# Kernel tuning notes

Hardware: AMD Instinct MI355X
Metric: run time of the kernel (lower is better)

Reference implementation:

```python
import jax, jax.numpy as jnp
import numpy as np

EPS_COS = 1e-8   # torch F.cosine_similarity eps
EPS_LN = 1e-6    # LayerNorm eps from source


def _attn_block(x, spat, roi, W, b, k):
    """MultiHeadedAttention_3 (flag=1) forward.
    x: [B,N,C], spat: [B,N,2], roi: [B,N,N], W: [h, 2C+4], b: [h].
    query[b,i,j]=x[b,j], key[b,i,j]=x[b,i]; ft = cat(query,key,spat_q,spat_k).
    The linear over the concat is split into per-part einsums (same math,
    avoids materializing the [B,N,N,2C+4] tensor).
    Returns attn1 * roi * topk-scatter mask, shape [B,N,N,h] (dims b,i,j,h).
    """
    B, N, C = x.shape
    Wq, Wk = W[:, :C], W[:, C:2 * C]
    Wsq, Wsk = W[:, 2 * C:2 * C + 2], W[:, 2 * C + 2:]
    qt = jnp.einsum('bjc,hc->bjh', x, Wq) + jnp.einsum('bjs,hs->bjh', spat, Wsq)
    kt = jnp.einsum('bic,hc->bih', x, Wk) + jnp.einsum('bis,hs->bih', spat, Wsk)
    logits = qt[:, None, :, :] + kt[:, :, None, :] + b  # [B,i,j,h]
    attn1 = jax.nn.sigmoid(logits)
    # relu(cosine_similarity(query, key, dim=3)) -> [B,i,j] (symmetric)
    xn = x / jnp.maximum(jnp.linalg.norm(x, axis=-1, keepdims=True), EPS_COS)
    scores = jax.nn.relu(jnp.einsum('bic,bjc->bij', xn, xn))
    # torch: atten_mask[:, :, idces, :] = 1.0 with idces [B,N,k,1] sets, for ALL
    # b,i,h, column j to 1 whenever j appears anywhere in idces (global scatter).
    _, idx = jax.lax.top_k(scores, k)  # [B,N,k]
    present = jnp.zeros((N,), x.dtype).at[idx.reshape(-1)].set(1.0)
    return attn1 * roi[:, :, :, None] * present[None, None, :, None]


def _gconv_relu(x, w, bias):
    """Grouped 1x1 Conv1d + ReLU. x: [B,Cin,N], w: [g, Cout/g, Cin/g]."""
    B, Cin, N = x.shape
    g, og, ig = w.shape
    y = jnp.einsum('bgin,goi->bgon', x.reshape(B, g, ig, N), w)
    return jax.nn.relu(y.reshape(B, g * og, N) + bias[None, :, None])


def _forward(input, masks_roi, score_mask, spat, W1, b1, W2, b2,
             cw1, cb1, cw2, cb2, ln_g, ln_b, node_num):
    B, N, C = input.shape
    h = W1.shape[0]
    masks = masks_roi * score_mask[:, None, :]
    f = (score_mask == 0).astype(input.dtype)          # [B,N]
    f_mask = f[:, :, None] * jnp.eye(N, dtype=input.dtype)  # diag_embed

    A1 = (_attn_block(input, spat, masks, W1, b1, node_num)
          + f_mask[:, :, :, None]) / 4.0               # [B,i,j,h]

    out1 = _gconv_relu(jnp.swapaxes(input, 1, 2), cw1, cb1)  # [B,mid,N]
    mid = out1.shape[1]
    # torch: matmul(out1.view(B,h,mid/h,N), A1.permute(0,3,2,1))  ([B,h,j,i])
    out1m = jnp.einsum('bhdj,bijh->bhdi', out1.reshape(B, h, mid // h, N), A1)
    out1 = out1 + out1m.reshape(B, mid, N)

    x2 = jnp.swapaxes(out1, 1, 2)                      # [B,N,mid]
    A2 = (_attn_block(x2, spat, masks, W2, b2, node_num)
          + f_mask[:, :, :, None]) / 4.0

    out2 = _gconv_relu(out1, cw2, cb2)                 # [B,out,N]
    co = out2.shape[1]
    out2m = jnp.einsum('bhdj,bijh->bhdi', out2.reshape(B, h, co // h, N), A2)
    out2m = jnp.swapaxes(out2m.reshape(B, co, N), 1, 2)  # [B,N,out]
    mu = jnp.mean(out2m, axis=-1, keepdims=True)
    var = jnp.mean(jnp.square(out2m - mu), axis=-1, keepdims=True)
    out2m = (out2m - mu) / jnp.sqrt(var + EPS_LN) * ln_g + ln_b
    out2 = out2 + jnp.swapaxes(out2m, 1, 2)
    return jnp.swapaxes(out2, 1, 2)                    # [B,N,out]


def setup_inputs() -> dict:
    key = jax.random.key(0)
    ks = jax.random.split(key, 10)
    B, N, C, MID, OUT, H, G = 8, 1024, 256, 256, 256, 4, 4
    s = 0.05
    return {
        'input': jax.random.normal(ks[0], (B, N, C), jnp.float32),
        'masks_roi': jax.random.randint(ks[1], (B, N, N), 0, 2).astype(jnp.float32),
        'score_mask': jax.random.randint(ks[2], (B, N), 0, 2).astype(jnp.float32),
        'spat': jax.random.uniform(ks[3], (B, N, 2), jnp.float32),
        'W1': s * jax.random.normal(ks[4], (H, 2 * C + 4), jnp.float32),
        'b1': jnp.zeros((H,), jnp.float32),
        'W2': s * jax.random.normal(ks[5], (H, 2 * MID + 4), jnp.float32),
        'b2': jnp.zeros((H,), jnp.float32),
        'cw1': s * jax.random.normal(ks[6], (G, MID // G, C // G), jnp.float32),
        'cb1': jnp.zeros((MID,), jnp.float32),
        'cw2': s * jax.random.normal(ks[7], (G, OUT // G, MID // G), jnp.float32),
        'cb2': jnp.zeros((OUT,), jnp.float32),
        'ln_g': jnp.ones((OUT,), jnp.float32),
        'ln_b': jnp.zeros((OUT,), jnp.float32),
        'node_num': 16,
    }


def reference(input, masks_roi, score_mask, spat, W1, b1, W2, b2,
              cw1, cb1, cw2, cb2, ln_g, ln_b, node_num):
    return _forward(input, masks_roi, score_mask, spat, W1, b1, W2, b2,
                    cw1, cb1, cw2, cb2, ln_g, ln_b, node_num)
```

## Files before the change

kernel.cpp:

```cpp
#include <hip/hip_runtime.h>

constexpr int Bb = 8;
constexpr int Nn = 1024;
constexpr int Cc = 256;
constexpr int Hh = 4;
constexpr int WROW = 2 * Cc + 4;

typedef float fx4 __attribute__((ext_vector_type(4)));
typedef float f32x4 __attribute__((ext_vector_type(4)));
typedef __bf16 bf16x8 __attribute__((ext_vector_type(8)));

#define GLL16(src, dst)                                                      \
  __builtin_amdgcn_global_load_lds(                                          \
      (const __attribute__((address_space(1))) void*)(src),                  \
      (__attribute__((address_space(3))) void*)(dst), 16, 0, 0)

__global__ __launch_bounds__(256) void k_roipack2(const float* __restrict__ roi,
                                                  const float* __restrict__ sm,
                                                  unsigned long long* __restrict__ roib,
                                                  int* __restrict__ cntb) {
  __shared__ short jmapS[1024];
  __shared__ unsigned char m4S[4][256];
  __shared__ int cntS;
  const int t = threadIdx.x, w = t >> 6, l = t & 63;
  const int gid = blockIdx.x * 4 + w;
  const int b = gid >> 10;

  if (w == 0) {
    int base = 0;
#pragma unroll
    for (int jc = 0; jc < 16; ++jc) {
      const int j = jc * 64 + l;
      const bool act = sm[b * Nn + j] != 0.f;
      const unsigned long long m = __ballot(act);
      if (act) jmapS[base + __popcll(m & ((1ull << l) - 1))] = (short)j;
      base += __popcll(m);
    }
    if (l == 0) {
      cntS = base;
      if ((blockIdx.x & 255) == 0) cntb[b] = base;
    }
  }

  {
    const fx4* r4 = (const fx4*)(roi + (size_t)gid * Nn);
#pragma unroll
    for (int k = 0; k < 4; ++k) {
      fx4 v = r4[k * 64 + l];
      unsigned nb = (v[0] != 0.f ? 1u : 0u) | (v[1] != 0.f ? 2u : 0u) |
                    (v[2] != 0.f ? 4u : 0u) | (v[3] != 0.f ? 8u : 0u);
      m4S[w][k * 64 + l] = (unsigned char)nb;
    }
  }
  __syncthreads();

  const int cnt = cntS;
  unsigned long long* orow = roib + (size_t)gid * 16;
#pragma unroll 4
  for (int pc = 0; pc < 16; ++pc) {
    const int idx = pc * 64 + l;
    const bool valid = idx < cnt;
    const int j = valid ? (int)jmapS[idx] : 0;
    const bool bit = valid && ((m4S[w][j >> 2] >> (j & 3)) & 1);
    unsigned long long m = __ballot(bit);
    if (l == 0) orow[pc] = m;
  }
}

template <int STAGE>
__global__ __launch_bounds__(256) void k_gconvq(const float* __restrict__ src,
                                                const float* __restrict__ cw,
                                                const float* __restrict__ cb,
                                                const float* __restrict__ sm,
                                                const float* __restrict__ spat,
                                                const float* __restrict__ W,
                                                const float* __restrict__ bias,
                                                float* __restrict__ out,
                                                __bf16* __restrict__ gsm,
                                                float* __restrict__ qt,
                                                float* __restrict__ kt) {
  __shared__ __align__(16) bf16x8 xsB[32][32];
  __shared__ float cbS[256];
  __shared__ float smS[32];
  __shared__ int pcolS[32];
  __shared__ int actS[32];
  const int b = blockIdx.x, tile = blockIdx.y;
  const int n0 = tile * 32;
  const int t = threadIdx.x, w = t >> 6, l = t & 63;

  if (w == 0) {
    const int fullc = n0 >> 6;
    int cbase = 0;
    unsigned long long am = 0;
    for (int jc = 0; jc <= fullc; ++jc) {
      unsigned long long m = __ballot(sm[b * Nn + jc * 64 + l] != 0.f);
      if (jc < fullc) cbase += __popcll(m); else am = m;
    }
    const int lsel = l - (n0 & 63);
    if (lsel >= 0 && lsel < 32) {
      pcolS[lsel] = cbase + __popcll(am & ((1ull << l) - 1));
      actS[lsel] = (int)((am >> l) & 1);
      smS[lsel] = 0.25f * sm[b * Nn + n0 + lsel];
    }
  }
  cbS[t] = cb[t];

  if (STAGE == 0) {
    const int n = t >> 3, c0 = (t & 7) * 32;
    const float* srow = src + ((size_t)(b * Nn + n0 + n)) * Cc + c0;
#pragma unroll
    for (int k = 0; k < 4; ++k) {
      fx4 v0 = *(const fx4*)&srow[k * 8];
      fx4 v1 = *(const fx4*)&srow[k * 8 + 4];
      bf16x8 bv;
#pragma unroll
      for (int e = 0; e < 4; ++e) { bv[e] = (__bf16)v0[e]; bv[4 + e] = (__bf16)v1[e]; }
      xsB[n][((c0 >> 3) + k) ^ (n & 7)] = bv;
    }
  } else {
#pragma unroll
    for (int rr = 0; rr < 8; ++rr) {
      const int c = rr * 32 + (t >> 3);
      const int nq = (t & 7) * 4;
      fx4 v = *(const fx4*)&src[((size_t)(b * Cc + c)) * Nn + n0 + nq];
#pragma unroll
      for (int j = 0; j < 4; ++j) {
        const int n = nq + j;
        __bf16* row = (__bf16*)&xsB[n][(c >> 3) ^ (n & 7)];
        row[c & 7] = (__bf16)v[j];
      }
    }
  }
  __syncthreads();

  const int g = w, dl = l & 15, q = l >> 4;

  bf16x8 a[4][2];
#pragma unroll
  for (int of = 0; of < 4; ++of)
#pragma unroll
    for (int ks = 0; ks < 2; ++ks) {
      const float* cwp = cw + ((size_t)(g * 64 + of * 16 + dl)) * 64 + ks * 32 + q * 8;
      fx4 c0 = *(const fx4*)cwp;
      fx4 c1 = *(const fx4*)(cwp + 4);
#pragma unroll
      for (int e = 0; e < 4; ++e) { a[of][ks][e] = (__bf16)c0[e]; a[of][ks][4 + e] = (__bf16)c1[e]; }
    }
  f32x4 acc[4][2] = {};
#pragma unroll
  for (int nf = 0; nf < 2; ++nf) {
    const int n = nf * 16 + dl;
#pragma unroll
    for (int ks = 0; ks < 2; ++ks) {
      bf16x8 bv = xsB[n][(g * 8 + ks * 4 + q) ^ (n & 7)];
#pragma unroll
      for (int of = 0; of < 4; ++of)
        acc[of][nf] = __builtin_amdgcn_mfma_f32_16x16x32_bf16(a[of][ks], bv, acc[of][nf], 0, 0, 0);
    }
  }
#pragma unroll
  for (int of = 0; of < 4; ++of)
#pragma unroll
    for (int nf = 0; nf < 2; ++nf) {
      const int n = nf * 16 + dl;
      const float smv = smS[n];
      const int act = actS[n];
      const int pc = pcolS[n];
#pragma unroll
      for (int r = 0; r < 4; ++r) {
        const int co = g * 64 + of * 16 + 4 * q + r;
        const float val = fmaxf(acc[of][nf][r] + cbS[co], 0.f);
        const size_t orow = ((size_t)(b * Cc + co)) * Nn;
        out[orow + n0 + n] = val;
        if (act) gsm[orow + pc] = (__bf16)(smv * val);
      }
    }

  {
    const int nl = l & 31, half = l >> 5;
    const float* wq = W + g * WROW;
    const float* wk = wq + Cc;
    float qa = 0.f, ka = 0.f;
#pragma unroll 8
    for (int c2 = 0; c2 < 64; ++c2) {
      const int c = half * 128 + c2 * 2;
      const __bf16* p = (const __bf16*)&xsB[nl][(c >> 3) ^ (nl & 7)] + (c & 7);
      const float x0 = (float)p[0], x1 = (float)p[1];
      qa = fmaf(x0, wq[c], fmaf(x1, wq[c + 1], qa));
      ka = fmaf(x0, wk[c], fmaf(x1, wk[c + 1], ka));
    }
    qa += __shfl_xor(qa, 32, 64);
    ka += __shfl_xor(ka, 32, 64);
    if (l < 32) {
      const int n = n0 + nl;
      const float s0 = spat[(b * Nn + n) * 2 + 0];
      const float s1 = spat[(b * Nn + n) * 2 + 1];
      const float* wsp = W + g * WROW + 2 * Cc;
      const float qf = qa + s0 * wsp[0] + s1 * wsp[1] + bias[g];
      const float kf = ka + s0 * wsp[2] + s1 * wsp[3];
      kt[(b * Hh + g) * Nn + n] = kf * -1.44269504f;
      if (actS[nl]) qt[(b * Hh + g) * Nn + pcolS[nl]] = qf * -1.44269504f;
    }
  }
}

template <int MODE>
__global__ __launch_bounds__(512, 4) void k_apply7(const float* __restrict__ g,
                                                   const __bf16* __restrict__ gsm,
                                                   const float* __restrict__ qt,
                                                   const float* __restrict__ kt,
                                                   const unsigned char* __restrict__ roib,
                                                   const float* __restrict__ sm,
                                                   const int* __restrict__ cntb,
                                                   float* __restrict__ out) {
  __shared__ __align__(16) __bf16 Bs[2][3][2][2048];
  __shared__ __align__(16) float qts[1024];
  __shared__ __align__(16) unsigned char rbs[64 * 128];
  const int b = blockIdx.x, it = blockIdx.y, h = blockIdx.z;
  const int t = threadIdx.x, w = t >> 6, l = t & 63;
  const int grp = w >> 2, wq = w & 3;
  const int i0 = it * 64;
  const int dl = l & 15, q = l >> 4, jqf = q * 8;
  const int iA = i0 + wq * 16 + dl;

  const float kvn = kt[(b * Hh + h) * Nn + iA];
  const float* smrow = sm + b * Nn;

  const int cnt = cntb[b];
  const int stepsTot = (cnt + 63) >> 6;
  const int S = (stepsTot + 1) >> 1;
  const int c0 = grp * S;

  const __bf16* gsrc = gsm + ((size_t)(b * Cc + h * 64 + wq * 16 + (l >> 2))) * Nn
                       + c0 * 64 + (l & 3) * 8;
  __bf16* ring = &Bs[grp][0][0][0];
  const int wdst = wq * 512;

  {
    const float2 qv = *(const float2*)&qt[(b * Hh + h) * Nn + t * 2];
    qts[t * 2 + 0] = qv.x;
    qts[t * 2 + 1] = qv.y;
  }
  {
    const int r = t >> 3, c = (t & 7) * 16;
    const char* src = (const char*)roib + ((size_t)(b * Nn + i0 + r)) * 128 + c;
    *(int4*)&rbs[r * 128 + c] = *(const int4*)src;
  }
  GLL16(gsrc, ring + 0 * 4096 + 0 * 2048 + wdst);
  GLL16(gsrc + 32, ring + 0 * 4096 + 1 * 2048 + wdst);
  GLL16(gsrc + 64, ring + 1 * 4096 + 0 * 2048 + wdst);
  GLL16(gsrc + 96, ring + 1 * 4096 + 1 * 2048 + wdst);
  __syncthreads();

  const int rbbase = (wq * 16 + dl) * 128;
  f32x4 acc[4] = {};
  int cur = 0;

  for (int s = 0; s < S; ++s) {
    const int ck = c0 + s;
    const unsigned int rb0 = rbs[rbbase + ck * 8 + q];
    const unsigned int rb1 = rbs[rbbase + ck * 8 + 4 + q];
    bf16x8 af0, af1;
    {
      fx4 qa = *(const fx4*)&qts[ck * 64 + jqf];
      fx4 qb = *(const fx4*)&qts[ck * 64 + jqf + 4];
#pragma unroll
      for (int e = 0; e < 4; ++e) {
        float sg = __builtin_amdgcn_rcpf(1.f + __builtin_amdgcn_exp2f(qa[e] + kvn));
        af0[e] = (__bf16)(((rb0 >> e) & 1) ? sg : 0.f);
      }
#pragma unroll
      for (int e = 0; e < 4; ++e) {
        float sg = __builtin_amdgcn_rcpf(1.f + __builtin_amdgcn_exp2f(qb[e] + kvn));
        af0[4 + e] = (__bf16)(((rb0 >> (4 + e)) & 1) ? sg : 0.f);
      }
      fx4 qc = *(const fx4*)&qts[ck * 64 + 32 + jqf];
      fx4 qd = *(const fx4*)&qts[ck * 64 + 32 + jqf + 4];
#pragma unroll
      for (int e = 0; e < 4; ++e) {
        float sg = __builtin_amdgcn_rcpf(1.f + __builtin_amdgcn_exp2f(qc[e] + kvn));
        af1[e] = (__bf16)(((rb1 >> e) & 1) ? sg : 0.f);
      }
#pragma unroll
      for (int e = 0; e < 4; ++e) {
        float sg = __builtin_amdgcn_rcpf(1.f + __builtin_amdgcn_exp2f(qd[e] + kvn));
        af1[4 + e] = (__bf16)(((rb1 >> (4 + e)) & 1) ? sg : 0.f);
      }
    }
    asm volatile("s_waitcnt vmcnt(2)\n\ts_barrier" ::: "memory");
    __builtin_amdgcn_sched_barrier(0);
    {
      const int nc = s + 2;
      const int off = (nc < S) ? nc * 64 : 0;
      const int pf = (cur == 0) ? 2 : cur - 1;
      GLL16(gsrc + off, ring + pf * 4096 + 0 * 2048 + wdst);
      GLL16(gsrc + off + 32, ring + pf * 4096 + 1 * 2048 + wdst);
    }
    const __bf16* bp = ring + cur * 4096;
#pragma unroll
    for (int nf = 0; nf < 4; ++nf) {
      bf16x8 bv = *(const bf16x8*)(bp + (nf * 16 + dl) * 32 + jqf);
      acc[nf] = __builtin_amdgcn_mfma_f32_16x16x32_bf16(af0, bv, acc[nf], 0, 0, 0);
    }
#pragma unroll
    for (int nf = 0; nf < 4; ++nf) {
      bf16x8 bv = *(const bf16x8*)(bp + 2048 + (nf * 16 + dl) * 32 + jqf);
      acc[nf] = __builtin_amdgcn_mfma_f32_16x16x32_bf16(af1, bv, acc[nf], 0, 0, 0);
    }
    cur = (cur == 2) ? 0 : cur + 1;
  }

  __syncthreads();
  float* accS = (float*)&Bs[0][0][0][0];
  if (grp == 1) {
#pragma unroll
    for (int nf = 0; nf < 4; ++nf)
      *(f32x4*)&accS[((wq * 64 + l) * 4 + nf) * 4] = acc[nf];
  }
  __syncthreads();
  if (grp == 0) {
#pragma unroll
    for (int nf = 0; nf < 4; ++nf)
      acc[nf] += *(const f32x4*)&accS[((wq * 64 + l) * 4 + nf) * 4];

    const int iw = i0 + wq * 16 + (l >> 4) * 4;
    fx4 sv = *(const fx4*)&smrow[iw];
    float fv[4];
#pragma unroll
    for (int r = 0; r < 4; ++r) fv[r] = (sv[r] == 0.f) ? 0.25f : 0.f;
    if (MODE == 0) {
#pragma unroll
      for (int nf = 0; nf < 4; ++nf) {
        const int ch = h * 64 + nf * 16 + dl;
        const size_t base = ((size_t)(b * Cc + ch)) * Nn + iw;
        fx4 gv = *(const fx4*)&g[base];
        fx4 res;
#pragma unroll
        for (int r = 0; r < 4; ++r) res[r] = gv[r] * (1.f + fv[r]) + acc[nf][r];
        *(fx4*)&out[base] = res;
      }
    } else {
#pragma unroll
      for (int nf = 0; nf < 4; ++nf) {
        const int ch = h * 64 + nf * 16 + dl;
        fx4 gv = *(const fx4*)&g[((size_t)(b * Cc + ch)) * Nn + iw];
#pragma unroll
        for (int r = 0; r < 4; ++r)
          out[((size_t)b * Nn + iw + r) * Cc + ch] = acc[nf][r] + fv[r] * gv[r];
      }
    }
  }
}

__global__ __launch_bounds__(256) void k_lnfinal(float* __restrict__ io,
                                                 const float* __restrict__ g2,
                                                 const float* __restrict__ lng,
                                                 const float* __restrict__ lnb) {
  __shared__ float gt[32][258];
  const int b = blockIdx.x, i0 = blockIdx.y * 32;
  const int t = threadIdx.x, w = t >> 6, l = t & 63;
  {
    const int n = t & 31, ch = t >> 5;
#pragma unroll 8
    for (int rr = 0; rr < 32; ++rr) {
      int c = rr * 8 + ch;
      gt[n][c] = g2[((size_t)(b * Cc + c)) * Nn + i0 + n];
    }
  }
  __syncthreads();
  const fx4 lngv = *(const fx4*)&lng[l * 4];
  const fx4 lnbv = *(const fx4*)&lnb[l * 4];
#pragma unroll
  for (int r = 0; r < 8; ++r) {
    const int n = r * 4 + w;
    const size_t base = ((size_t)(b * Nn) + i0 + n) * Cc + l * 4;
    fx4 v = *(const fx4*)&io[base];
    float s = v[0] + v[1] + v[2] + v[3];
    float sq = v[0] * v[0] + v[1] * v[1] + v[2] * v[2] + v[3] * v[3];
#pragma unroll
    for (int off = 32; off; off >>= 1) {
      s += __shfl_xor(s, off, 64);
      sq += __shfl_xor(sq, off, 64);
    }
    const float m = s * (1.f / 256.f);
    const float var = sq * (1.f / 256.f) - m * m;
    const float rstd = rsqrtf(fmaxf(var, 0.f) + 1e-6f);
    fx4 gv = *(const fx4*)&gt[n][l * 4];
    fx4 res;
#pragma unroll
    for (int e = 0; e < 4; ++e)
      res[e] = gv[e] + (v[e] - m) * rstd * lngv[e] + lnbv[e];
    *(fx4*)&io[base] = res;
  }
}

extern "C" void kernel_launch(void* const* d_in, const int* in_sizes, int n_in,
                              void* d_out, int out_size, void* d_ws, size_t ws_size,
                              hipStream_t stream) {
  (void)in_sizes; (void)n_in; (void)out_size; (void)ws_size;
  const float* input = (const float*)d_in[0];
  const float* roi   = (const float*)d_in[1];
  const float* sm    = (const float*)d_in[2];
  const float* spat  = (const float*)d_in[3];
  const float* W1    = (const float*)d_in[4];
  const float* b1    = (const float*)d_in[5];
  const float* W2    = (const float*)d_in[6];
  const float* b2    = (const float*)d_in[7];
  const float* cw1   = (const float*)d_in[8];
  const float* cb1   = (const float*)d_in[9];
  const float* cw2   = (const float*)d_in[10];
  const float* cb2   = (const float*)d_in[11];
  const float* lng   = (const float*)d_in[12];
  const float* lnb   = (const float*)d_in[13];

  float* outf = (float*)d_out;
  char* ws = (char*)d_ws;
  const size_t PLANE = (size_t)Bb * Cc * Nn;
  float* gbuf = (float*)ws;
  __bf16* gsm = (__bf16*)(ws + PLANE * 4);
  unsigned long long* roib =
      (unsigned long long*)(ws + PLANE * 4 + PLANE * 2);
  float* qtb = (float*)((char*)roib + (size_t)Bb * Nn * 128);
  float* ktb = qtb + Bb * Hh * Nn;
  int* cntb = (int*)(ktb + Bb * Hh * Nn);
  float* out1 = outf;

  k_roipack2<<<dim3(2048), 256, 0, stream>>>(roi, sm, roib, cntb);
  k_gconvq<0><<<dim3(8, 32), 256, 0, stream>>>(input, cw1, cb1, sm, spat, W1, b1,
                                               gbuf, gsm, qtb, ktb);
  k_apply7<0><<<dim3(8, 16, 4), 512, 0, stream>>>(gbuf, gsm, qtb, ktb,
                                                  (const unsigned char*)roib, sm,
                                                  cntb, out1);
  k_gconvq<1><<<dim3(8, 32), 256, 0, stream>>>(out1, cw2, cb2, sm, spat, W2, b2,
                                               gbuf, gsm, qtb, ktb);
  k_apply7<1><<<dim3(8, 16, 4), 512, 0, stream>>>(gbuf, gsm, qtb, ktb,
                                                  (const unsigned char*)roib, sm,
                                                  cntb, outf);
  k_lnfinal<<<dim3(8, 32), 256, 0, stream>>>(outf, gbuf, lng, lnb);
}
```

Baseline: 74.30 us.

## Store stage-1 output node-major and stage q/k weights in shared memory

The first apply kernel now writes its output in [B,N,C] layout, the same as the final output, so the second grouped-conv kernel can use the coalesced row-major load path instead of the transposed channel-major gather. The q/k projection weights are staged into shared memory, and the projection loop reads bf16x8 vectors from the tile rather than scalar global weights. The barrier is moved after the weight-fragment loads to overlap them with the tile fill. The stage-1 store becomes strided across channels, which may cost more write bandwidth.

Result: no change. 74.62 us (+0.4%).

```diff
diff --git a/kernel.cpp b/kernel.cpp
--- a/kernel.cpp
+++ b/kernel.cpp
@@ -41,7 +41,6 @@
       if ((blockIdx.x & 255) == 0) cntb[b] = base;
     }
   }
-
   {
     const fx4* r4 = (const fx4*)(roi + (size_t)gid * Nn);
 #pragma unroll
@@ -53,7 +52,6 @@
     }
   }
   __syncthreads();
-
   const int cnt = cntS;
   unsigned long long* orow = roib + (size_t)gid * 16;
 #pragma unroll 4
@@ -67,7 +65,6 @@
   }
 }
 
-template <int STAGE>
 __global__ __launch_bounds__(256) void k_gconvq(const float* __restrict__ src,
                                                 const float* __restrict__ cw,
                                                 const float* __restrict__ cb,
@@ -80,6 +77,7 @@
                                                 float* __restrict__ qt,
                                                 float* __restrict__ kt) {
   __shared__ __align__(16) bf16x8 xsB[32][32];
+  __shared__ __align__(16) float WqkS[8][256];
   __shared__ float cbS[256];
   __shared__ float smS[32];
   __shared__ int pcolS[32];
@@ -104,8 +102,12 @@
     }
   }
   cbS[t] = cb[t];
-
-  if (STAGE == 0) {
+  for (int idx = t; idx < 2048; idx += 256) {
+    const int row = idx >> 8, c = idx & 255;
+    WqkS[row][c] = W[(row >> 1) * WROW + (row & 1) * Cc + c];
+  }
+
+  {
     const int n = t >> 3, c0 = (t & 7) * 32;
     const float* srow = src + ((size_t)(b * Nn + n0 + n)) * Cc + c0;
 #pragma unroll
@@ -117,21 +119,7 @@
       for (int e = 0; e < 4; ++e) { bv[e] = (__bf16)v0[e]; bv[4 + e] = (__bf16)v1[e]; }
       xsB[n][((c0 >> 3) + k) ^ (n & 7)] = bv;
     }
-  } else {
-#pragma unroll
-    for (int rr = 0; rr < 8; ++rr) {
-      const int c = rr * 32 + (t >> 3);
-      const int nq = (t & 7) * 4;
-      fx4 v = *(const fx4*)&src[((size_t)(b * Cc + c)) * Nn + n0 + nq];
-#pragma unroll
-      for (int j = 0; j < 4; ++j) {
-        const int n = nq + j;
-        __bf16* row = (__bf16*)&xsB[n][(c >> 3) ^ (n & 7)];
-        row[c & 7] = (__bf16)v[j];
-      }
-    }
-  }
-  __syncthreads();
+  }
 
   const int g = w, dl = l & 15, q = l >> 4;
 
@@ -146,6 +134,8 @@
 #pragma unroll
       for (int e = 0; e < 4; ++e) { a[of][ks][e] = (__bf16)c0[e]; a[of][ks][4 + e] = (__bf16)c1[e]; }
     }
+  __syncthreads();
+
   f32x4 acc[4][2] = {};
 #pragma unroll
   for (int nf = 0; nf < 2; ++nf) {
@@ -178,16 +168,18 @@
 
   {
     const int nl = l & 31, half = l >> 5;
-    const float* wq = W + g * WROW;
-    const float* wk = wq + Cc;
     float qa = 0.f, ka = 0.f;
-#pragma unroll 8
-    for (int c2 = 0; c2 < 64; ++c2) {
-      const int c = half * 128 + c2 * 2;
-      const __bf16* p = (const __bf16*)&xsB[nl][(c >> 3) ^ (nl & 7)] + (c & 7);
-      const float x0 = (float)p[0], x1 = (float)p[1];
-      qa = fmaf(x0, wq[c], fmaf(x1, wq[c + 1], qa));
-      ka = fmaf(x0, wk[c], fmaf(x1, wk[c + 1], ka));
+#pragma unroll
+    for (int k = 0; k < 16; ++k) {
+      bf16x8 bv = xsB[nl][(half * 16 + k) ^ (nl & 7)];
+      const float* wqp = &WqkS[g * 2 + 0][half * 128 + k * 8];
+      const float* wkp = &WqkS[g * 2 + 1][half * 128 + k * 8];
+#pragma unroll
+      for (int e = 0; e < 8; ++e) {
+        const float x = (float)bv[e];
+        qa = fmaf(x, wqp[e], qa);
+        ka = fmaf(x, wkp[e], ka);
+      }
     }
     qa += __shfl_xor(qa, 32, 64);
     ka += __shfl_xor(ka, 32, 64);
@@ -235,6 +227,7 @@
                        + c0 * 64 + (l & 3) * 8;
   __bf16* ring = &Bs[grp][0][0][0];
   const int wdst = wq * 512;
+  const int rbbase = (wq * 16 + dl) * 128;
 
   {
     const float2 qv = *(const float2*)&qt[(b * Hh + h) * Nn + t * 2];
@@ -252,7 +245,6 @@
   GLL16(gsrc + 96, ring + 1 * 4096 + 1 * 2048 + wdst);
   __syncthreads();
 
-  const int rbbase = (wq * 16 + dl) * 128;
   f32x4 acc[4] = {};
   int cur = 0;
 
@@ -328,25 +320,15 @@
     float fv[4];
 #pragma unroll
     for (int r = 0; r < 4; ++r) fv[r] = (sv[r] == 0.f) ? 0.25f : 0.f;
-    if (MODE == 0) {
-#pragma unroll
-      for (int nf = 0; nf < 4; ++nf) {
-        const int ch = h * 64 + nf * 16 + dl;
-        const size_t base = ((size_t)(b * Cc + ch)) * Nn + iw;
-        fx4 gv = *(const fx4*)&g[base];
-        fx4 res;
-#pragma unroll
-        for (int r = 0; r < 4; ++r) res[r] = gv[r] * (1.f + fv[r]) + acc[nf][r];
-        *(fx4*)&out[base] = res;
-      }
-    } else {
-#pragma unroll
-      for (int nf = 0; nf < 4; ++nf) {
-        const int ch = h * 64 + nf * 16 + dl;
-        fx4 gv = *(const fx4*)&g[((size_t)(b * Cc + ch)) * Nn + iw];
-#pragma unroll
-        for (int r = 0; r < 4; ++r)
-          out[((size_t)b * Nn + iw + r) * Cc + ch] = acc[nf][r] + fv[r] * gv[r];
+#pragma unroll
+    for (int nf = 0; nf < 4; ++nf) {
+      const int ch = h * 64 + nf * 16 + dl;
+      fx4 gv = *(const fx4*)&g[((size_t)(b * Cc + ch)) * Nn + iw];
+#pragma unroll
+      for (int r = 0; r < 4; ++r) {
+        const float res = (MODE == 0) ? gv[r] * (1.f + fv[r]) + acc[nf][r]
+                                      : acc[nf][r] + fv[r] * gv[r];
+        out[((size_t)b * Nn + iw + r) * Cc + ch] = res;
       }
     }
   }
@@ -426,13 +408,13 @@
   float* out1 = outf;
 
   k_roipack2<<<dim3(2048), 256, 0, stream>>>(roi, sm, roib, cntb);
-  k_gconvq<0><<<dim3(8, 32), 256, 0, stream>>>(input, cw1, cb1, sm, spat, W1, b1,
-                                               gbuf, gsm, qtb, ktb);
+  k_gconvq<<<dim3(8, 32), 256, 0, stream>>>(input, cw1, cb1, sm, spat, W1, b1,
+                                            gbuf, gsm, qtb, ktb);
   k_apply7<0><<<dim3(8, 16, 4), 512, 0, stream>>>(gbuf, gsm, qtb, ktb,
                                                   (const unsigned char*)roib, sm,
                                                   cntb, out1);
-  k_gconvq<1><<<dim3(8, 32), 256, 0, stream>>>(out1, cw2, cb2, sm, spat, W2, b2,
-                                               gbuf, gsm, qtb, ktb);
+  k_gconvq<<<dim3(8, 32), 256, 0, stream>>>(out1, cw2, cb2, sm, spat, W2, b2,
+                                            gbuf, gsm, qtb, ktb);
   k_apply7<1><<<dim3(8, 16, 4), 512, 0, stream>>>(gbuf, gsm, qtb, ktb,
                                                   (const unsigned char*)roib, sm,
                                                   cntb, outf);
```
